# Kernel optimization log

Hardware: AMD Instinct MI355X
Metric: run time of the kernel (lower is better)

## Reference

```python
import jax, jax.numpy as jnp
import numpy as np


def setup_inputs() -> dict:
    key = jax.random.key(0)
    ks = jax.random.split(key, 5)
    B, H, W, C = 4, 64, 64, 256
    Ck = C // 8  # key/query channels = 32
    x = jax.random.normal(ks[0], (B, H, W, C), dtype=jnp.float32)
    # 1x1 conv kernels (spec_norm=False -> plain conv), Glorot-ish scaling
    Wf = jax.random.normal(ks[1], (C, Ck), dtype=jnp.float32) * (1.0 / np.sqrt(C))
    Wg = jax.random.normal(ks[2], (C, Ck), dtype=jnp.float32) * (1.0 / np.sqrt(C))
    Wh = jax.random.normal(ks[3], (C, C), dtype=jnp.float32) * (1.0 / np.sqrt(C))
    bf = jnp.zeros((Ck,), dtype=jnp.float32)
    bg = jnp.zeros((Ck,), dtype=jnp.float32)
    bh = jnp.zeros((C,), dtype=jnp.float32)
    # gamma is zero-init in the module; use a nonzero value so the attention
    # branch actually contributes to the output (as after some training).
    gamma = jnp.float32(0.5)
    return {"x": x, "Wf": Wf, "bf": bf, "Wg": Wg, "bg": bg,
            "Wh": Wh, "bh": bh, "gamma": gamma}


def reference(x, Wf, bf, Wg, bg, Wh, bh, gamma):
    B, H, W, C = x.shape
    N = H * W
    xf = x.reshape(B, N, C)  # hw_flatten of input (1x1 conv == per-pixel matmul)
    f = xf @ Wf + bf         # [B, N, Ck] keys
    g = xf @ Wg + bg         # [B, N, Ck] queries
    h = xf @ Wh + bh         # [B, N, C]  values
    s = jnp.einsum('bqk,bnk->bqn', g, f)  # [B, N, N] scores (g @ f^T)
    b = jax.nn.softmax(s, axis=-1)
    o = jnp.einsum('bqn,bnc->bqc', b, h)  # [B, N, C]
    # in-channels == nfilters, so scale(x) = x (identity)
    y = gamma * o.reshape(B, H, W, C) + x
    return y
```

## Files before the change

kernel.cpp:

```cpp
#include <hip/hip_runtime.h>
#include <stdint.h>

#define B_ 4
#define N_ 4096
#define C_ 256
#define LOG2E 1.44269504088896340736f
#define SOFT_OFF 88.0f

typedef float f32x4 __attribute__((ext_vector_type(4)));
typedef float f32x16 __attribute__((ext_vector_type(16)));
typedef short s16x8 __attribute__((ext_vector_type(8)));
typedef __bf16 bf16x8 __attribute__((ext_vector_type(8)));
typedef _Float16 f16x8 __attribute__((ext_vector_type(8)));

static __device__ __forceinline__ unsigned short f2bf(float f) {
    union { float f; uint32_t u; } v; v.f = f;
    return (unsigned short)((v.u + 0x7FFFu + ((v.u >> 16) & 1u)) >> 16);
}
static __device__ __forceinline__ unsigned short f2bf_rh(float f) {
    union { float f; uint32_t u; } v; v.f = f;
    return (unsigned short)((v.u + 0x8000u) >> 16);
}

__global__ __launch_bounds__(256) void wprep(
    const float* __restrict__ Wf, const float* __restrict__ Wg,
    const float* __restrict__ Wh, _Float16* __restrict__ WT)
{
    __shared__ float tile[64][33];
    const int t = blockIdx.x, kc = blockIdx.y, tid = threadIdx.x;
    const float* src; int stride;
    if (t == 0)      { src = Wf;                stride = 32;  }
    else if (t == 1) { src = Wg;                stride = 32;  }
    else             { src = Wh + (t - 2) * 32; stride = 256; }

    const int c = tid & 31, a = tid >> 5;
    #pragma unroll
    for (int p = 0; p < 8; p++) {
        int kk = p * 8 + a;
        tile[kk][c] = src[(size_t)(kc * 64 + kk) * stride + c];
    }
    __syncthreads();
    const int kk = tid & 63, aa = tid >> 6;
    #pragma unroll
    for (int p = 0; p < 8; p++) {
        int cc = p * 4 + aa;
        WT[(size_t)(t * 32 + cc) * 256 + kc * 64 + kk] = (_Float16)tile[kk][cc];
    }
}

__global__ __launch_bounds__(256, 3) void proj_kernel(
    const float* __restrict__ x,
    const float* __restrict__ bfp, const float* __restrict__ bgp,
    const float* __restrict__ bhp,
    const _Float16* __restrict__ WT,
    _Float16* __restrict__ qf16, _Float16* __restrict__ kf16,
    unsigned short* __restrict__ v_frag)
{
    __shared__ __align__(16) _Float16 xs[64 * 256];
    __shared__ __align__(16) unsigned short tbuf[4][32 * 40];

    const int tid  = threadIdx.x;
    const int lane = tid & 63;
    const int wave = tid >> 6;
    const int m_   = lane & 31;
    const int k8   = lane >> 5;
    const int row0 = blockIdx.x * 64;
    const int b    = row0 >> 12;
    const int n0   = row0 & 4095;
    const int kt   = n0 >> 6;

    #pragma unroll
    for (int i = 0; i < 8; i++) {
        int r  = 8 * i + (tid >> 5);
        int c5 = tid & 31;
        const f32x4* src = (const f32x4*)(x + (size_t)(row0 + r) * 256 + c5 * 8);
        f32x4 a = src[0], c4 = src[1];
        f16x8 h = { (_Float16)a.x, (_Float16)a.y, (_Float16)a.z, (_Float16)a.w,
                    (_Float16)c4.x, (_Float16)c4.y, (_Float16)c4.z, (_Float16)c4.w };
        int chunk = (((r >> 5) * 32 + c5)) * 32 + ((r & 31) ^ (c5 & 7));
        *(f16x8*)(xs + chunk * 8) = h;
    }
    __syncthreads();

    const int rowsub = wave & 1;
    const int tile   = blockIdx.y * 2 + (wave >> 1);
    const _Float16* wb = WT + (size_t)(tile * 32 + m_) * 256 + k8 * 8;

    f32x16 acc;
    #pragma unroll
    for (int i = 0; i < 16; i++) acc[i] = 0.f;

    f16x8 Bb[2][4];
    #pragma unroll
    for (int j = 0; j < 4; j++) Bb[0][j] = *(const f16x8*)(wb + j * 16);
    #pragma unroll
    for (int g4 = 0; g4 < 4; g4++) {
        const int cur = g4 & 1, nxt = cur ^ 1;
        if (g4 < 3)
            #pragma unroll
            for (int j = 0; j < 4; j++)
                Bb[nxt][j] = *(const f16x8*)(wb + (g4 * 4 + 4 + j) * 16);
        #pragma unroll
        for (int j = 0; j < 4; j++) {
            int ks = g4 * 4 + j;
            f16x8 A = *(const f16x8*)(xs + ((rowsub * 32 + ks * 2 + k8) * 32
                                            + (m_ ^ ((ks * 2 + k8) & 7))) * 8);
            acc = __builtin_amdgcn_mfma_f32_32x32x16_f16(A, Bb[cur][j], acc, 0, 0, 0);
        }
    }

    if (tile < 2) {
        float bias = (tile == 0) ? bfp[m_] : bgp[m_];
        _Float16* dst = (tile == 0) ? kf16 : qf16;
        #pragma unroll
        for (int r = 0; r < 16; r++) {
            int m = (r & 3) + 8 * (r >> 2) + 4 * k8;
            int row = row0 + rowsub * 32 + m;
            dst[(size_t)row * 32 + m_] = (_Float16)(acc[r] + bias);
        }
    } else {
        const int ht   = tile - 2;
        const int chgv = ht >> 2, chslv = ht & 3;
        float bias = bhp[ht * 32 + m_];
        unsigned short* buf = tbuf[wave];
        #pragma unroll
        for (int u = 0; u < 8; u++) {
            int r = 2 * u;
            int m = (r & 3) + 8 * (r >> 2) + 4 * k8;
            uint32_t v = (uint32_t)f2bf(acc[r] + bias)
                       | ((uint32_t)f2bf(acc[r + 1] + bias) << 16);
            *(uint32_t*)(buf + m_ * 40 + m) = v;
        }
        #pragma unroll
        for (int u = 0; u < 2; u++) {
            int idx2 = u * 64 + lane;
            int chr = idx2 >> 2, q8 = idx2 & 3;
            s16x8 vv = *(const s16x8*)(buf + chr * 40 + q8 * 8);
            int oct = rowsub * 4 + q8;
            size_t e = (((((size_t)(b * 2 + chgv) * 64 + kt) * 8 + oct) * 4
                          + chslv) * 32 + chr) * 8;
            *(s16x8*)(v_frag + e) = vv;
        }
    }
}

__global__ __launch_bounds__(512, 4) void attn_kernel(
    const _Float16* __restrict__ qf16, const _Float16* __restrict__ kf16,
    const unsigned short* __restrict__ v_frag,
    const float* __restrict__ x, const float* __restrict__ gamma_p,
    float* __restrict__ out)
{
    __shared__ __align__(16) unsigned short P_s[2][2048];
    __shared__ float l_s[2][2][32];

    const int tid  = threadIdx.x;
    const int lane = tid & 63;
    const int wave = tid >> 6;
    const int qsub = wave & 1;
    const int chsl = wave >> 1;
    const int m_   = lane & 31;
    const int k8   = lane >> 5;
    const int qt   = blockIdx.x;
    const int chg  = blockIdx.y;
    const int b    = blockIdx.z;
    const size_t bn = (size_t)b * N_;
    const int ch0  = chg * 128;
    const bool is_s = (wave < 4);
    const int ksub  = wave >> 1;

    const unsigned short* vb = v_frag + (size_t)(b * 2 + chg) * 524288
                             + (size_t)k8 * 1024 + chsl * 256 + m_ * 8;

    f16x8 Aq0, Aq1, Kc0, Kc1;
    if (is_s) {
        const int qrow = qt * 64 + qsub * 32 + m_;
        Aq0 = *(const f16x8*)(qf16 + (bn + qrow) * 32 + k8 * 8);
        Aq1 = *(const f16x8*)(qf16 + (bn + qrow) * 32 + 16 + k8 * 8);
        const _Float16* kp = kf16 + (bn + ksub * 32 + m_) * 32;
        Kc0 = *(const f16x8*)(kp + k8 * 8);
        Kc1 = *(const f16x8*)(kp + 16 + k8 * 8);
    }

    f32x16 acc;
    float l_acc[16];
    #pragma unroll
    for (int i = 0; i < 16; i++) { acc[i] = 0.f; l_acc[i] = 0.f; }

    for (int kt = 0; kt < N_ / 64; kt++) {
        const int ktn = (kt < 63) ? kt + 1 : 63;
        bf16x8 Bv[4];
        #pragma unroll
        for (int kstep = 0; kstep < 4; kstep++)
            Bv[kstep] = *(const bf16x8*)(vb + (size_t)kt * 8192 + kstep * 2048);
        f16x8 Kn0, Kn1;
        if (is_s) {
            const _Float16* kp = kf16 + (bn + ktn * 64 + ksub * 32 + m_) * 32;
            Kn0 = *(const f16x8*)(kp + k8 * 8);
            Kn1 = *(const f16x8*)(kp + 16 + k8 * 8);
        }
        if (is_s) {
            f32x16 s;
            #pragma unroll
            for (int i = 0; i < 16; i++) s[i] = 0.f;
            s = __builtin_amdgcn_mfma_f32_32x32x16_f16(Aq0, Kc0, s, 0, 0, 0);
            s = __builtin_amdgcn_mfma_f32_32x32x16_f16(Aq1, Kc1, s, 0, 0, 0);
            unsigned short* Pb = P_s[qsub];
            const int octet = ksub * 4 + (m_ >> 3);
            const int kofs = m_ & 7;
            #pragma unroll
            for (int r = 0; r < 16; r++) {
                float p = __builtin_amdgcn_exp2f(fmaf(s[r], LOG2E, -SOFT_OFF));
                l_acc[r] += p;
                int m = (r & 3) + 8 * (r >> 2) + 4 * k8;
                Pb[(octet * 32 + (m ^ (octet & 3))) * 8 + kofs] = f2bf_rh(p);
            }
        }
        __syncthreads();

        const unsigned short* Pr = P_s[qsub];
        #pragma unroll
        for (int kstep = 0; kstep < 4; kstep++) {
            int oct = kstep * 2 + k8;
            bf16x8 Ap = *(const bf16x8*)(Pr + (oct * 32 + (m_ ^ (oct & 3))) * 8);
            acc = __builtin_amdgcn_mfma_f32_32x32x16_bf16(Ap, Bv[kstep], acc, 0, 0, 0);
        }
        if (is_s) { Kc0 = Kn0; Kc1 = Kn1; }
        __syncthreads();
    }

    if (is_s) {
        #pragma unroll
        for (int off = 1; off < 32; off <<= 1)
            #pragma unroll
            for (int r = 0; r < 16; r++)
                l_acc[r] += __shfl_xor(l_acc[r], off, 64);
        if (m_ == 0) {
            #pragma unroll
            for (int r = 0; r < 16; r++) {
                int q = (r & 3) + 8 * (r >> 2) + 4 * k8;
                l_s[qsub][ksub][q] = l_acc[r];
            }
        }
    }
    __syncthreads();

    const float gamma = *gamma_p;
    #pragma unroll
    for (int r = 0; r < 16; r++) {
        int q = (r & 3) + 8 * (r >> 2) + 4 * k8;
        float l = l_s[qsub][0][q] + l_s[qsub][1][q];
        size_t idx = (bn + qt * 64 + qsub * 32 + q) * 256 + ch0 + chsl * 32 + m_;
        out[idx] = gamma * (acc[r] / l) + x[idx];
    }
}

extern "C" void kernel_launch(void* const* d_in, const int* in_sizes, int n_in,
                              void* d_out, int out_size, void* d_ws, size_t ws_size,
                              hipStream_t stream) {
    const float* x   = (const float*)d_in[0];
    const float* Wf  = (const float*)d_in[1];
    const float* bfp = (const float*)d_in[2];
    const float* Wg  = (const float*)d_in[3];
    const float* bgp = (const float*)d_in[4];
    const float* Wh  = (const float*)d_in[5];
    const float* bhp = (const float*)d_in[6];
    const float* gam = (const float*)d_in[7];
    float* out = (float*)d_out;

    unsigned char* ws = (unsigned char*)d_ws;
    const size_t MB = 1 << 20;
    _Float16* WT    = (_Float16*)(ws);
    _Float16* qf16  = (_Float16*)(ws + 1 * MB);
    _Float16* kf16  = (_Float16*)(ws + 2 * MB);
    unsigned short* v_frag = (unsigned short*)(ws + 3 * MB);

    wprep<<<dim3(10, 4), dim3(256), 0, stream>>>(Wf, Wg, Wh, WT);
    proj_kernel<<<dim3(256, 5), dim3(256), 0, stream>>>(
        x, bfp, bgp, bhp, WT, qf16, kf16, v_frag);
    attn_kernel<<<dim3(64, 2, 4), dim3(512), 0, stream>>>(
        qf16, kf16, v_frag, x, gam, out);
}
```

Measured before the change: 158.7 us.

## Double-buffer P tile in LDS and prefetch V fragments one tile ahead

Adds a second LDS buffer for the probability tile so each iteration needs a single barrier instead of two. The V fragments for the next key tile are loaded into registers one iteration early, using two ping-ponged register sets in a loop unrolled by two. The raw s_waitcnt/s_barrier replaces __syncthreads. This should hide global load latency and cut barrier stalls, at the cost of more registers and LDS, which could lower occupancy at 4 blocks per CU.

```diff
diff --git a/kernel.cpp b/kernel.cpp
--- a/kernel.cpp
+++ b/kernel.cpp
@@ -144,13 +144,47 @@
     }
 }
 
+#define ATTN_STEP(KT, PAR, BCUR, BNXT, KC0, KC1, KN0, KN1)                       \
+    {                                                                            \
+        const int ktn_ = ((KT) < 63) ? (KT) + 1 : 63;                            \
+        _Pragma("unroll")                                                        \
+        for (int ks_ = 0; ks_ < 4; ks_++)                                        \
+            BNXT[ks_] = *(const bf16x8*)(vb + (size_t)ktn_ * 8192 + ks_ * 2048); \
+        if (is_s) {                                                              \
+            const _Float16* kp_ = kf16 + (bn + ktn_ * 64 + ksub * 32 + m_) * 32; \
+            KN0 = *(const f16x8*)(kp_ + k8 * 8);                                 \
+            KN1 = *(const f16x8*)(kp_ + 16 + k8 * 8);                            \
+            f32x16 s_;                                                           \
+            _Pragma("unroll")                                                    \
+            for (int i = 0; i < 16; i++) s_[i] = 0.f;                            \
+            s_ = __builtin_amdgcn_mfma_f32_32x32x16_f16(Aq0, KC0, s_, 0, 0, 0);  \
+            s_ = __builtin_amdgcn_mfma_f32_32x32x16_f16(Aq1, KC1, s_, 0, 0, 0);  \
+            unsigned short* Pb_ = P_s[qsub][PAR];                                \
+            _Pragma("unroll")                                                    \
+            for (int r = 0; r < 16; r++) {                                       \
+                float p_ = __builtin_amdgcn_exp2f(fmaf(s_[r], LOG2E, -SOFT_OFF));\
+                l_acc[r] += p_;                                                  \
+                int mi_ = (r & 3) + 8 * (r >> 2) + 4 * k8;                       \
+                Pb_[(octet * 32 + (mi_ ^ octsw)) * 8 + kofs] = f2bf_rh(p_);      \
+            }                                                                    \
+        }                                                                        \
+        __asm volatile("s_waitcnt lgkmcnt(0)\n\ts_barrier" ::: "memory");        \
+        const unsigned short* Pr_ = P_s[qsub][PAR];                              \
+        _Pragma("unroll")                                                        \
+        for (int ks_ = 0; ks_ < 4; ks_++) {                                      \
+            int oct_ = ks_ * 2 + k8;                                             \
+            bf16x8 Ap_ = *(const bf16x8*)(Pr_ + (oct_ * 32 + (m_ ^ (oct_ & 3))) * 8); \
+            acc = __builtin_amdgcn_mfma_f32_32x32x16_bf16(Ap_, BCUR[ks_], acc, 0, 0, 0); \
+        }                                                                        \
+    }
+
 __global__ __launch_bounds__(512, 4) void attn_kernel(
     const _Float16* __restrict__ qf16, const _Float16* __restrict__ kf16,
     const unsigned short* __restrict__ v_frag,
     const float* __restrict__ x, const float* __restrict__ gamma_p,
     float* __restrict__ out)
 {
-    __shared__ __align__(16) unsigned short P_s[2][2048];
+    __shared__ __align__(16) unsigned short P_s[2][2][2048];
     __shared__ float l_s[2][2][32];
 
     const int tid  = threadIdx.x;
@@ -167,65 +201,35 @@
     const int ch0  = chg * 128;
     const bool is_s = (wave < 4);
     const int ksub  = wave >> 1;
+    const int octet = ksub * 4 + (m_ >> 3);
+    const int octsw = octet & 3;
+    const int kofs  = m_ & 7;
 
     const unsigned short* vb = v_frag + (size_t)(b * 2 + chg) * 524288
                              + (size_t)k8 * 1024 + chsl * 256 + m_ * 8;
 
-    f16x8 Aq0, Aq1, Kc0, Kc1;
+    f16x8 Aq0 = {}, Aq1 = {}, Kca0 = {}, Kca1 = {}, Kcb0 = {}, Kcb1 = {};
     if (is_s) {
         const int qrow = qt * 64 + qsub * 32 + m_;
         Aq0 = *(const f16x8*)(qf16 + (bn + qrow) * 32 + k8 * 8);
         Aq1 = *(const f16x8*)(qf16 + (bn + qrow) * 32 + 16 + k8 * 8);
         const _Float16* kp = kf16 + (bn + ksub * 32 + m_) * 32;
-        Kc0 = *(const f16x8*)(kp + k8 * 8);
-        Kc1 = *(const f16x8*)(kp + 16 + k8 * 8);
-    }
+        Kca0 = *(const f16x8*)(kp + k8 * 8);
+        Kca1 = *(const f16x8*)(kp + 16 + k8 * 8);
+    }
+    bf16x8 Ba[4], Bb2[4];
+    #pragma unroll
+    for (int ks = 0; ks < 4; ks++)
+        Ba[ks] = *(const bf16x8*)(vb + ks * 2048);
 
     f32x16 acc;
     float l_acc[16];
     #pragma unroll
     for (int i = 0; i < 16; i++) { acc[i] = 0.f; l_acc[i] = 0.f; }
 
-    for (int kt = 0; kt < N_ / 64; kt++) {
-        const int ktn = (kt < 63) ? kt + 1 : 63;
-        bf16x8 Bv[4];
-        #pragma unroll
-        for (int kstep = 0; kstep < 4; kstep++)
-            Bv[kstep] = *(const bf16x8*)(vb + (size_t)kt * 8192 + kstep * 2048);
-        f16x8 Kn0, Kn1;
-        if (is_s) {
-            const _Float16* kp = kf16 + (bn + ktn * 64 + ksub * 32 + m_) * 32;
-            Kn0 = *(const f16x8*)(kp + k8 * 8);
-            Kn1 = *(const f16x8*)(kp + 16 + k8 * 8);
-        }
-        if (is_s) {
-            f32x16 s;
-            #pragma unroll
-            for (int i = 0; i < 16; i++) s[i] = 0.f;
-            s = __builtin_amdgcn_mfma_f32_32x32x16_f16(Aq0, Kc0, s, 0, 0, 0);
-            s = __builtin_amdgcn_mfma_f32_32x32x16_f16(Aq1, Kc1, s, 0, 0, 0);
-            unsigned short* Pb = P_s[qsub];
-            const int octet = ksub * 4 + (m_ >> 3);
-            const int kofs = m_ & 7;
-            #pragma unroll
-            for (int r = 0; r < 16; r++) {
-                float p = __builtin_amdgcn_exp2f(fmaf(s[r], LOG2E, -SOFT_OFF));
-                l_acc[r] += p;
-                int m = (r & 3) + 8 * (r >> 2) + 4 * k8;
-                Pb[(octet * 32 + (m ^ (octet & 3))) * 8 + kofs] = f2bf_rh(p);
-            }
-        }
-        __syncthreads();
-
-        const unsigned short* Pr = P_s[qsub];
-        #pragma unroll
-        for (int kstep = 0; kstep < 4; kstep++) {
-            int oct = kstep * 2 + k8;
-            bf16x8 Ap = *(const bf16x8*)(Pr + (oct * 32 + (m_ ^ (oct & 3))) * 8);
-            acc = __builtin_amdgcn_mfma_f32_32x32x16_bf16(Ap, Bv[kstep], acc, 0, 0, 0);
-        }
-        if (is_s) { Kc0 = Kn0; Kc1 = Kn1; }
-        __syncthreads();
+    for (int kt = 0; kt < 64; kt += 2) {
+        ATTN_STEP(kt,     0, Ba,  Bb2, Kca0, Kca1, Kcb0, Kcb1);
+        ATTN_STEP(kt + 1, 1, Bb2, Ba,  Kcb0, Kcb1, Kca0, Kca1);
     }
 
     if (is_s) {
```

Result: slower. 208.8 us (+31.6%).

## Spread score computation over all waves, double-buffer P, widen projection tiles

Applied to the files above, without the earlier changes.

In the attention kernel, all eight waves now compute scores and exponentials for a 128-key chunk per iteration, instead of only four waves doing it for 64 keys. The probability tile is double-buffered so each iteration needs one barrier instead of two, and row sums are combined over four partial sums. This is meant to remove the idle time of value-only waves and cut synchronization per key. The projection kernel now computes 2–3 output tiles per wave over a 2-wide grid, reusing the converted x tile in shared memory, at higher register cost and with a barrier inside a per-wave conditional loop, which makes barrier counts differ between waves.

```diff
diff --git a/kernel.cpp b/kernel.cpp
--- a/kernel.cpp
+++ b/kernel.cpp
@@ -48,7 +48,7 @@
     }
 }
 
-__global__ __launch_bounds__(256, 3) void proj_kernel(
+__global__ __launch_bounds__(256, 2) void proj_kernel(
     const float* __restrict__ x,
     const float* __restrict__ bfp, const float* __restrict__ bgp,
     const float* __restrict__ bhp,
@@ -65,6 +65,7 @@
     const int m_   = lane & 31;
     const int k8   = lane >> 5;
     const int row0 = blockIdx.x * 64;
+    const int half = blockIdx.y;
     const int b    = row0 >> 12;
     const int n0   = row0 & 4095;
     const int kt   = n0 >> 6;
@@ -83,63 +84,90 @@
     __syncthreads();
 
     const int rowsub = wave & 1;
-    const int tile   = blockIdx.y * 2 + (wave >> 1);
-    const _Float16* wb = WT + (size_t)(tile * 32 + m_) * 256 + k8 * 8;
-
-    f32x16 acc;
-    #pragma unroll
-    for (int i = 0; i < 16; i++) acc[i] = 0.f;
-
-    f16x8 Bb[2][4];
-    #pragma unroll
-    for (int j = 0; j < 4; j++) Bb[0][j] = *(const f16x8*)(wb + j * 16);
+    const int tg     = wave >> 1;
+    const int ntile  = (half == 0) ? 3 : 2;
+    const int t_base = (half == 0) ? tg * 3 : 6 + tg * 2;
+    const _Float16* wb[3];
+    #pragma unroll
+    for (int t = 0; t < 3; t++)
+        wb[t] = WT + (size_t)((t_base + (t < ntile ? t : 0)) * 32 + m_) * 256 + k8 * 8;
+
+    f32x16 acc[3];
+    #pragma unroll
+    for (int t = 0; t < 3; t++)
+        #pragma unroll
+        for (int i = 0; i < 16; i++) acc[t][i] = 0.f;
+
+    f16x8 Bb[2][4][3];
+    #pragma unroll
+    for (int j = 0; j < 4; j++)
+        #pragma unroll
+        for (int t = 0; t < 3; t++) {
+            if (t >= ntile) break;
+            Bb[0][j][t] = *(const f16x8*)(wb[t] + j * 16);
+        }
     #pragma unroll
     for (int g4 = 0; g4 < 4; g4++) {
         const int cur = g4 & 1, nxt = cur ^ 1;
         if (g4 < 3)
             #pragma unroll
             for (int j = 0; j < 4; j++)
-                Bb[nxt][j] = *(const f16x8*)(wb + (g4 * 4 + 4 + j) * 16);
+                #pragma unroll
+                for (int t = 0; t < 3; t++) {
+                    if (t >= ntile) break;
+                    Bb[nxt][j][t] = *(const f16x8*)(wb[t] + (g4 * 4 + 4 + j) * 16);
+                }
         #pragma unroll
         for (int j = 0; j < 4; j++) {
             int ks = g4 * 4 + j;
             f16x8 A = *(const f16x8*)(xs + ((rowsub * 32 + ks * 2 + k8) * 32
                                             + (m_ ^ ((ks * 2 + k8) & 7))) * 8);
-            acc = __builtin_amdgcn_mfma_f32_32x32x16_f16(A, Bb[cur][j], acc, 0, 0, 0);
-        }
-    }
-
-    if (tile < 2) {
-        float bias = (tile == 0) ? bfp[m_] : bgp[m_];
-        _Float16* dst = (tile == 0) ? kf16 : qf16;
-        #pragma unroll
-        for (int r = 0; r < 16; r++) {
-            int m = (r & 3) + 8 * (r >> 2) + 4 * k8;
-            int row = row0 + rowsub * 32 + m;
-            dst[(size_t)row * 32 + m_] = (_Float16)(acc[r] + bias);
-        }
-    } else {
-        const int ht   = tile - 2;
-        const int chgv = ht >> 2, chslv = ht & 3;
-        float bias = bhp[ht * 32 + m_];
-        unsigned short* buf = tbuf[wave];
-        #pragma unroll
-        for (int u = 0; u < 8; u++) {
-            int r = 2 * u;
-            int m = (r & 3) + 8 * (r >> 2) + 4 * k8;
-            uint32_t v = (uint32_t)f2bf(acc[r] + bias)
-                       | ((uint32_t)f2bf(acc[r + 1] + bias) << 16);
-            *(uint32_t*)(buf + m_ * 40 + m) = v;
-        }
-        #pragma unroll
-        for (int u = 0; u < 2; u++) {
-            int idx2 = u * 64 + lane;
-            int chr = idx2 >> 2, q8 = idx2 & 3;
-            s16x8 vv = *(const s16x8*)(buf + chr * 40 + q8 * 8);
-            int oct = rowsub * 4 + q8;
-            size_t e = (((((size_t)(b * 2 + chgv) * 64 + kt) * 8 + oct) * 4
-                          + chslv) * 32 + chr) * 8;
-            *(s16x8*)(v_frag + e) = vv;
+            #pragma unroll
+            for (int t = 0; t < 3; t++) {
+                if (t >= ntile) break;
+                acc[t] = __builtin_amdgcn_mfma_f32_32x32x16_f16(A, Bb[cur][j][t],
+                                                                acc[t], 0, 0, 0);
+            }
+        }
+    }
+
+    #pragma unroll
+    for (int t = 0; t < 3; t++) {
+        if (t >= ntile) break;
+        const int tile = t_base + t;
+        if (tile < 2) {
+            float bias = (tile == 0) ? bfp[m_] : bgp[m_];
+            _Float16* dst = (tile == 0) ? kf16 : qf16;
+            #pragma unroll
+            for (int r = 0; r < 16; r++) {
+                int m = (r & 3) + 8 * (r >> 2) + 4 * k8;
+                int row = row0 + rowsub * 32 + m;
+                dst[(size_t)row * 32 + m_] = (_Float16)(acc[t][r] + bias);
+            }
+        } else {
+            const int ht   = tile - 2;
+            const int chgv = ht >> 2, chslv = ht & 3;
+            float bias = bhp[ht * 32 + m_];
+            unsigned short* buf = tbuf[wave];
+            #pragma unroll
+            for (int u = 0; u < 8; u++) {
+                int r = 2 * u;
+                int m = (r & 3) + 8 * (r >> 2) + 4 * k8;
+                uint32_t v = (uint32_t)f2bf(acc[t][r] + bias)
+                           | ((uint32_t)f2bf(acc[t][r + 1] + bias) << 16);
+                *(uint32_t*)(buf + m_ * 40 + m) = v;
+            }
+            #pragma unroll
+            for (int u = 0; u < 2; u++) {
+                int idx2 = u * 64 + lane;
+                int chr = idx2 >> 2, q8 = idx2 & 3;
+                s16x8 vv = *(const s16x8*)(buf + chr * 40 + q8 * 8);
+                int oct = rowsub * 4 + q8;
+                size_t e = (((((size_t)(b * 2 + chgv) * 64 + kt) * 8 + oct) * 4
+                              + chslv) * 32 + chr) * 8;
+                *(s16x8*)(v_frag + e) = vv;
+            }
+            __syncthreads();
         }
     }
 }
@@ -150,14 +178,14 @@
     const float* __restrict__ x, const float* __restrict__ gamma_p,
     float* __restrict__ out)
 {
-    __shared__ __align__(16) unsigned short P_s[2][2048];
-    __shared__ float l_s[2][2][32];
+    __shared__ __align__(16) unsigned short P_s[2][2][4096];
+    __shared__ float l_s[2][4][32];
 
     const int tid  = threadIdx.x;
     const int lane = tid & 63;
     const int wave = tid >> 6;
     const int qsub = wave & 1;
-    const int chsl = wave >> 1;
+    const int j    = wave >> 1;
     const int m_   = lane & 31;
     const int k8   = lane >> 5;
     const int qt   = blockIdx.x;
@@ -165,81 +193,79 @@
     const int b    = blockIdx.z;
     const size_t bn = (size_t)b * N_;
     const int ch0  = chg * 128;
-    const bool is_s = (wave < 4);
-    const int ksub  = wave >> 1;
+    const int octw = j * 4 + (m_ >> 3);
+    const int osw  = octw & 3;
+    const int kofs = m_ & 7;
 
     const unsigned short* vb = v_frag + (size_t)(b * 2 + chg) * 524288
-                             + (size_t)k8 * 1024 + chsl * 256 + m_ * 8;
-
-    f16x8 Aq0, Aq1, Kc0, Kc1;
-    if (is_s) {
-        const int qrow = qt * 64 + qsub * 32 + m_;
-        Aq0 = *(const f16x8*)(qf16 + (bn + qrow) * 32 + k8 * 8);
-        Aq1 = *(const f16x8*)(qf16 + (bn + qrow) * 32 + 16 + k8 * 8);
-        const _Float16* kp = kf16 + (bn + ksub * 32 + m_) * 32;
-        Kc0 = *(const f16x8*)(kp + k8 * 8);
-        Kc1 = *(const f16x8*)(kp + 16 + k8 * 8);
-    }
+                             + (size_t)k8 * 1024 + j * 256 + m_ * 8;
+
+    const int qrow = qt * 64 + qsub * 32 + m_;
+    const f16x8 Aq0 = *(const f16x8*)(qf16 + (bn + qrow) * 32 + k8 * 8);
+    const f16x8 Aq1 = *(const f16x8*)(qf16 + (bn + qrow) * 32 + 16 + k8 * 8);
+
+    const _Float16* kp0 = kf16 + (bn + j * 32 + m_) * 32;
+    f16x8 Kc0 = *(const f16x8*)(kp0 + k8 * 8);
+    f16x8 Kc1 = *(const f16x8*)(kp0 + 16 + k8 * 8);
 
     f32x16 acc;
     float l_acc[16];
     #pragma unroll
     for (int i = 0; i < 16; i++) { acc[i] = 0.f; l_acc[i] = 0.f; }
 
-    for (int kt = 0; kt < N_ / 64; kt++) {
-        const int ktn = (kt < 63) ? kt + 1 : 63;
-        bf16x8 Bv[4];
-        #pragma unroll
-        for (int kstep = 0; kstep < 4; kstep++)
-            Bv[kstep] = *(const bf16x8*)(vb + (size_t)kt * 8192 + kstep * 2048);
-        f16x8 Kn0, Kn1;
-        if (is_s) {
-            const _Float16* kp = kf16 + (bn + ktn * 64 + ksub * 32 + m_) * 32;
-            Kn0 = *(const f16x8*)(kp + k8 * 8);
-            Kn1 = *(const f16x8*)(kp + 16 + k8 * 8);
-        }
-        if (is_s) {
-            f32x16 s;
-            #pragma unroll
-            for (int i = 0; i < 16; i++) s[i] = 0.f;
-            s = __builtin_amdgcn_mfma_f32_32x32x16_f16(Aq0, Kc0, s, 0, 0, 0);
-            s = __builtin_amdgcn_mfma_f32_32x32x16_f16(Aq1, Kc1, s, 0, 0, 0);
-            unsigned short* Pb = P_s[qsub];
-            const int octet = ksub * 4 + (m_ >> 3);
-            const int kofs = m_ & 7;
-            #pragma unroll
-            for (int r = 0; r < 16; r++) {
-                float p = __builtin_amdgcn_exp2f(fmaf(s[r], LOG2E, -SOFT_OFF));
-                l_acc[r] += p;
-                int m = (r & 3) + 8 * (r >> 2) + 4 * k8;
-                Pb[(octet * 32 + (m ^ (octet & 3))) * 8 + kofs] = f2bf_rh(p);
-            }
+    for (int it = 0; it < 32; it++) {
+        const int par = it & 1;
+        bf16x8 Bv[8];
+        #pragma unroll
+        for (int t64 = 0; t64 < 2; t64++)
+            #pragma unroll
+            for (int ks = 0; ks < 4; ks++)
+                Bv[t64 * 4 + ks] = *(const bf16x8*)(vb
+                    + (size_t)(it * 2 + t64) * 8192 + ks * 2048);
+        const int itn = (it < 31) ? it + 1 : 31;
+        const _Float16* kpn = kf16 + (bn + itn * 128 + j * 32 + m_) * 32;
+        f16x8 Kn0 = *(const f16x8*)(kpn + k8 * 8);
+        f16x8 Kn1 = *(const f16x8*)(kpn + 16 + k8 * 8);
+
+        f32x16 s;
+        #pragma unroll
+        for (int i = 0; i < 16; i++) s[i] = 0.f;
+        s = __builtin_amdgcn_mfma_f32_32x32x16_f16(Aq0, Kc0, s, 0, 0, 0);
+        s = __builtin_amdgcn_mfma_f32_32x32x16_f16(Aq1, Kc1, s, 0, 0, 0);
+
+        unsigned short* Pb = P_s[par][qsub];
+        #pragma unroll
+        for (int r = 0; r < 16; r++) {
+            float p = __builtin_amdgcn_exp2f(fmaf(s[r], LOG2E, -SOFT_OFF));
+            l_acc[r] += p;
+            int q = (r & 3) + 8 * (r >> 2) + 4 * k8;
+            Pb[(octw * 32 + (q ^ osw)) * 8 + kofs] = f2bf_rh(p);
         }
         __syncthreads();
 
-        const unsigned short* Pr = P_s[qsub];
-        #pragma unroll
-        for (int kstep = 0; kstep < 4; kstep++) {
-            int oct = kstep * 2 + k8;
-            bf16x8 Ap = *(const bf16x8*)(Pr + (oct * 32 + (m_ ^ (oct & 3))) * 8);
-            acc = __builtin_amdgcn_mfma_f32_32x32x16_bf16(Ap, Bv[kstep], acc, 0, 0, 0);
-        }
-        if (is_s) { Kc0 = Kn0; Kc1 = Kn1; }
-        __syncthreads();
-    }
-
-    if (is_s) {
-        #pragma unroll
-        for (int off = 1; off < 32; off <<= 1)
-            #pragma unroll
-            for (int r = 0; r < 16; r++)
-                l_acc[r] += __shfl_xor(l_acc[r], off, 64);
-        if (m_ == 0) {
-            #pragma unroll
-            for (int r = 0; r < 16; r++) {
-                int q = (r & 3) + 8 * (r >> 2) + 4 * k8;
-                l_s[qsub][ksub][q] = l_acc[r];
-            }
+        const unsigned short* Pr = P_s[par][qsub];
+        #pragma unroll
+        for (int t64 = 0; t64 < 2; t64++)
+            #pragma unroll
+            for (int ks = 0; ks < 4; ks++) {
+                int oct = t64 * 8 + ks * 2 + k8;
+                bf16x8 Ap = *(const bf16x8*)(Pr + (oct * 32 + (m_ ^ (oct & 3))) * 8);
+                acc = __builtin_amdgcn_mfma_f32_32x32x16_bf16(Ap, Bv[t64 * 4 + ks],
+                                                              acc, 0, 0, 0);
+            }
+        Kc0 = Kn0; Kc1 = Kn1;
+    }
+
+    #pragma unroll
+    for (int off = 1; off < 32; off <<= 1)
+        #pragma unroll
+        for (int r = 0; r < 16; r++)
+            l_acc[r] += __shfl_xor(l_acc[r], off, 64);
+    if (m_ == 0) {
+        #pragma unroll
+        for (int r = 0; r < 16; r++) {
+            int q = (r & 3) + 8 * (r >> 2) + 4 * k8;
+            l_s[qsub][j][q] = l_acc[r];
         }
     }
     __syncthreads();
@@ -248,8 +274,9 @@
     #pragma unroll
     for (int r = 0; r < 16; r++) {
         int q = (r & 3) + 8 * (r >> 2) + 4 * k8;
-        float l = l_s[qsub][0][q] + l_s[qsub][1][q];
-        size_t idx = (bn + qt * 64 + qsub * 32 + q) * 256 + ch0 + chsl * 32 + m_;
+        float l = l_s[qsub][0][q] + l_s[qsub][1][q]
+                + l_s[qsub][2][q] + l_s[qsub][3][q];
+        size_t idx = (bn + qt * 64 + qsub * 32 + q) * 256 + ch0 + j * 32 + m_;
         out[idx] = gamma * (acc[r] / l) + x[idx];
     }
 }
@@ -275,7 +302,7 @@
     unsigned short* v_frag = (unsigned short*)(ws + 3 * MB);
 
     wprep<<<dim3(10, 4), dim3(256), 0, stream>>>(Wf, Wg, Wh, WT);
-    proj_kernel<<<dim3(256, 5), dim3(256), 0, stream>>>(
+    proj_kernel<<<dim3(256, 2), dim3(256), 0, stream>>>(
         x, bfp, bgp, bhp, WT, qf16, kf16, v_frag);
     attn_kernel<<<dim3(64, 2, 4), dim3(512), 0, stream>>>(
         qf16, kf16, v_frag, x, gam, out);
```

New measurement: 172.6 us. +8.8%, slower.
